# Kernel tuning notes

Hardware: AMD Instinct MI355X
Metric: run time of the kernel (lower is better)

## Reference

```python
import jax, jax.numpy as jnp
import numpy as np
from jax import lax

D_MODEL = 1024
D_STATE = 16


def setup_inputs() -> dict:
    key = jax.random.key(0)
    ks = jax.random.split(key, 7)
    B, L = 4, 2048
    x = jax.random.normal(ks[0], (B, L, D_MODEL), dtype=jnp.float32)
    s = 1.0 / np.sqrt(D_MODEL)
    W_dt = jax.random.uniform(ks[1], (D_MODEL, D_MODEL), jnp.float32, -s, s)
    b_dt = jax.random.uniform(ks[2], (D_MODEL,), jnp.float32, -s, s)
    W_B = jax.random.uniform(ks[3], (D_STATE, D_MODEL), jnp.float32, -s, s)
    W_C = jax.random.uniform(ks[4], (D_STATE, D_MODEL), jnp.float32, -s, s)
    A = jax.random.normal(ks[5], (D_MODEL, D_STATE), dtype=jnp.float32)
    A_log = jnp.log(jnp.abs(A) + 1e-4)
    D = jnp.ones((D_MODEL,), dtype=jnp.float32)
    return {"x": x, "W_dt": W_dt, "b_dt": b_dt, "W_B": W_B, "W_C": W_C,
            "A_log": A_log, "D": D}


def reference(x, W_dt, b_dt, W_B, W_C, A_log, D):
    B, L, Dm = x.shape
    N = A_log.shape[1]
    dt = jax.nn.softplus(jnp.einsum('bld,ed->ble', x, W_dt) + b_dt)  # [B,L,D]
    Bp = jnp.einsum('bld,nd->bln', x, W_B)   # [B,L,N]
    Cp = jnp.einsum('bld,nd->bln', x, W_C)   # [B,L,N]
    A = -jnp.exp(A_log)                      # [D,N]
    dA = jnp.exp(dt[..., None] * A)          # [B,L,D,N]
    # fuse dB * x: dB[bldn] = dt*Bp; input term = dB * x
    dBx = dt[..., None] * Bp[:, :, None, :] * x[..., None]  # [B,L,D,N]

    def step(h, inp):
        dA_t, dBx_t, C_t, x_t = inp
        h = dA_t * h + dBx_t                              # [B,D,N]
        y = jnp.einsum('bdn,bn->bd', h, C_t) + D * x_t    # [B,D]
        return h, y

    h0 = jnp.zeros((B, Dm, N), dtype=x.dtype)
    xs = (jnp.swapaxes(dA, 0, 1), jnp.swapaxes(dBx, 0, 1),
          jnp.swapaxes(Cp, 0, 1), jnp.swapaxes(x, 0, 1))
    _, ys = lax.scan(step, h0, xs)           # ys: [L,B,D]
    return jnp.swapaxes(ys, 0, 1)            # [B,L,D]
```

## Files before the change

### kernel.cpp

```cpp
#include <hip/hip_runtime.h>
#include <hip/hip_bf16.h>
#include <math.h>

#define DM 1024
#define DS 16
#define BB 4
#define LL 2048
#define LC 32
#define NC (LL/LC)
#define MT 8192
#define NT64 16
#define NCT 17

typedef __attribute__((ext_vector_type(8))) short short8;
typedef __attribute__((ext_vector_type(4))) float floatx4;

__device__ __forceinline__ float softplus_fast(float v) {
  return fmaxf(v, 0.f) + __logf(1.f + __expf(-fabsf(v)));
}

__global__ __launch_bounds__(256) void convert_kernel(
    const float* __restrict__ X, const float* __restrict__ W_dt,
    const float* __restrict__ WB, const float* __restrict__ WC,
    __hip_bfloat16* __restrict__ Xb, __hip_bfloat16* __restrict__ Wx)
{
  const size_t i  = (size_t)blockIdx.x * 256 + threadIdx.x;
  const size_t NX = (size_t)MT * DM / 8;
  const size_t NW = (size_t)DM * DM / 8;
  const size_t NB = (size_t)DS * DM / 8;
  const float* src;
  __hip_bfloat16* dst;
  size_t u;
  if (i < NX)                { src = X;    dst = Xb;                        u = i; }
  else if (i < NX + NW)      { src = W_dt; dst = Wx;                        u = i - NX; }
  else if (i < NX + NW + NB) { src = WB;   dst = Wx + (size_t)1024 * DM;    u = i - NX - NW; }
  else if (i < NX + NW + 2 * NB) { src = WC; dst = Wx + (size_t)1040 * DM;  u = i - NX - NW - NB; }
  else {
    const size_t z = i - NX - NW - 2 * NB;
    const short8 zz = {0, 0, 0, 0, 0, 0, 0, 0};
    *(short8*)&Wx[(size_t)1056 * DM + z * 8] = zz;
    return;
  }
  const float4 a = *(const float4*)&src[u * 8];
  const float4 b = *(const float4*)&src[u * 8 + 4];
  union { short8 v; __hip_bfloat16 h[8]; } o;
  o.h[0] = __float2bfloat16(a.x); o.h[1] = __float2bfloat16(a.y);
  o.h[2] = __float2bfloat16(a.z); o.h[3] = __float2bfloat16(a.w);
  o.h[4] = __float2bfloat16(b.x); o.h[5] = __float2bfloat16(b.y);
  o.h[6] = __float2bfloat16(b.z); o.h[7] = __float2bfloat16(b.w);
  *(short8*)&dst[u * 8] = o.v;
}

__global__ __launch_bounds__(256) void gemm_dt_mfma(
    const __hip_bfloat16* __restrict__ Xb, const __hip_bfloat16* __restrict__ Wx,
    const float* __restrict__ bias, __hip_bfloat16* __restrict__ DTb,
    float* __restrict__ BP, float* __restrict__ CP)
{
  __shared__ short As[3][128 * 64];
  __shared__ short Bs[3][64 * 64];
  const int tid  = threadIdx.x;
  const int lane = tid & 63;
  const int wid  = tid >> 6;
  const int wm   = wid >> 1, wn = wid & 1;

  const int bid  = blockIdx.x;
  const int tile = (bid & 7) * 136 + (bid >> 3);
  const int row0 = (tile / NCT) * 128;
  const int col0 = (tile % NCT) * 64;

  const floatx4 zero = {0.f, 0.f, 0.f, 0.f};
  floatx4 acc[4][2];
#pragma unroll
  for (int i = 0; i < 4; ++i)
#pragma unroll
    for (int j = 0; j < 2; ++j) acc[i][j] = zero;

  auto STAGE = [&](int buf, int t) {
    const int k0 = t * 64;
#pragma unroll
    for (int q = 0; q < 4; ++q) {
      const int fe = q * 256 + tid;
      const int r  = fe >> 3;
      const int kk = (fe & 7) ^ (r & 7);
      __builtin_amdgcn_global_load_lds(
          (const __attribute__((address_space(1))) void*)&Xb[(size_t)(row0 + r) * DM + k0 + kk * 8],
          (__attribute__((address_space(3))) void*)&As[buf][fe * 8], 16, 0, 0);
    }
#pragma unroll
    for (int q = 0; q < 2; ++q) {
      const int fe = q * 256 + tid;
      const int r  = fe >> 3;
      const int kk = (fe & 7) ^ (r & 7);
      __builtin_amdgcn_global_load_lds(
          (const __attribute__((address_space(1))) void*)&Wx[(size_t)(col0 + r) * DM + k0 + kk * 8],
          (__attribute__((address_space(3))) void*)&Bs[buf][fe * 8], 16, 0, 0);
    }
  };

  const int fr = lane & 15;
  const int ks = lane >> 4;

  STAGE(0, 0);
  STAGE(1, 1);
  int cur = 0;
  for (int t = 0; t < NT64; ++t) {
    if (t < NT64 - 1) asm volatile("s_waitcnt vmcnt(6)" ::: "memory");
    else              asm volatile("s_waitcnt vmcnt(0)" ::: "memory");
    __builtin_amdgcn_s_barrier();
    __builtin_amdgcn_sched_barrier(0);

    int c2 = cur + 2; if (c2 >= 3) c2 -= 3;
    if (t + 2 < NT64) STAGE(c2, t + 2);

    short8 af[4][2], bfr[2][2];
#pragma unroll
    for (int i = 0; i < 4; ++i) {
      const int ar = wm * 64 + i * 16 + fr;
#pragma unroll
      for (int s = 0; s < 2; ++s) {
        const int ch = (ks + 4 * s) ^ (ar & 7);
        af[i][s] = *(const short8*)&As[cur][ar * 64 + ch * 8];
      }
    }
#pragma unroll
    for (int j = 0; j < 2; ++j) {
      const int br = wn * 32 + j * 16 + fr;
#pragma unroll
      for (int s = 0; s < 2; ++s) {
        const int ch = (ks + 4 * s) ^ (br & 7);
        bfr[j][s] = *(const short8*)&Bs[cur][br * 64 + ch * 8];
      }
    }
#pragma unroll
    for (int s = 0; s < 2; ++s)
#pragma unroll
      for (int i = 0; i < 4; ++i)
#pragma unroll
        for (int j = 0; j < 2; ++j)
          acc[i][j] = __builtin_amdgcn_mfma_f32_16x16x32_bf16(af[i][s], bfr[j][s], acc[i][j], 0, 0, 0);

    cur += 1; if (cur >= 3) cur -= 3;
  }

  const int cl = lane & 15;
  const int rg = lane >> 4;
  if (col0 < 1024) {
#pragma unroll
    for (int i = 0; i < 4; ++i) {
#pragma unroll
      for (int r = 0; r < 4; ++r) {
        const size_t row = (size_t)(row0 + wm * 64 + i * 16 + rg * 4 + r);
#pragma unroll
        for (int j = 0; j < 2; ++j) {
          const int col = col0 + wn * 32 + j * 16 + cl;
          const float v = acc[i][j][r] + bias[col];
          DTb[row * DM + col] = __float2bfloat16(softplus_fast(v));
        }
      }
    }
  } else if (wn == 0) {
#pragma unroll
    for (int i = 0; i < 4; ++i) {
#pragma unroll
      for (int r = 0; r < 4; ++r) {
        const size_t row = (size_t)(row0 + wm * 64 + i * 16 + rg * 4 + r);
        BP[row * DS + cl] = acc[i][0][r];
        CP[row * DS + cl] = acc[i][1][r];
      }
    }
  }
}

__global__ __launch_bounds__(256) void scan_partial_kernel(
    const __hip_bfloat16* __restrict__ DT, const __hip_bfloat16* __restrict__ X,
    const float* __restrict__ Bp, const float* __restrict__ A_log,
    float* __restrict__ SD, float* __restrict__ HP)
{
  const int d = blockIdx.x * 256 + threadIdx.x;
  const int c = blockIdx.y;
  const int b = blockIdx.z;
  float A[DS], h[DS];
  float sdt = 0.f;
  const float4* arow = (const float4*)&A_log[(size_t)d * DS];
#pragma unroll
  for (int m = 0; m < 4; ++m) {
    const float4 a4 = arow[m];
    A[m*4+0] = -__expf(a4.x); A[m*4+1] = -__expf(a4.y);
    A[m*4+2] = -__expf(a4.z); A[m*4+3] = -__expf(a4.w);
  }
#pragma unroll
  for (int n = 0; n < DS; ++n) h[n] = 0.f;

  const int l0 = c * LC;
  size_t idx = ((size_t)b * LL + l0) * DM + d;
  const float4* bv = (const float4*)&Bp[((size_t)b * LL + l0) * DS];

  float dtb[4], xb[4];
#pragma unroll
  for (int u = 0; u < 4; ++u) {
    dtb[u] = __bfloat162float(DT[idx + (size_t)u * DM]);
    xb[u]  = __bfloat162float(X[idx + (size_t)u * DM]);
  }

  for (int l = 0; l < LC; l += 4) {
    float dtn[4], xn[4];
    if (l + 4 < LC) {
#pragma unroll
      for (int u = 0; u < 4; ++u) {
        dtn[u] = __bfloat162float(DT[idx + (size_t)(u + 4) * DM]);
        xn[u]  = __bfloat162float(X[idx + (size_t)(u + 4) * DM]);
      }
    }
#pragma unroll
    for (int u = 0; u < 4; ++u) {
      const float dtv = dtb[u], xv = xb[u];
      const float dx = dtv * xv;
      sdt += dtv;
      const float4 b0 = bv[(l+u)*4+0], b1 = bv[(l+u)*4+1];
      const float4 b2 = bv[(l+u)*4+2], b3 = bv[(l+u)*4+3];
      const float bb[DS] = {b0.x,b0.y,b0.z,b0.w, b1.x,b1.y,b1.z,b1.w,
                            b2.x,b2.y,b2.z,b2.w, b3.x,b3.y,b3.z,b3.w};
#pragma unroll
      for (int n = 0; n < DS; ++n) {
        const float dA = __expf(dtv * A[n]);
        h[n] = fmaf(dA, h[n], dx * bb[n]);
      }
    }
    idx += (size_t)4 * DM;
#pragma unroll
    for (int u = 0; u < 4; ++u) { dtb[u] = dtn[u]; xb[u] = xn[u]; }
  }
  SD[((size_t)b * NC + c) * DM + d] = sdt;
  const size_t o = (((size_t)b * NC + c) * DM + d) * DS;
  float4* hp = (float4*)&HP[o];
#pragma unroll
  for (int m = 0; m < 4; ++m)
    hp[m] = make_float4(h[m*4+0], h[m*4+1], h[m*4+2], h[m*4+3]);
}

__global__ __launch_bounds__(256) void combine_kernel(
    const float* __restrict__ SD, const float* __restrict__ A_log,
    float* HP)
{
  const int idx = blockIdx.x * 256 + threadIdx.x;
  const int b  = idx >> 14;
  const int dn = idx & 16383;
  const int d  = dn >> 4;
  const float A = -__expf(A_log[dn]);
  float h = 0.f;
#pragma unroll 4
  for (int c = 0; c < NC; ++c) {
    const size_t o = (((size_t)b * NC + c) << 14) + dn;
    const float p  = __expf(SD[((size_t)b * NC + c) * DM + d] * A);
    const float hp = HP[o];
    HP[o] = h;
    h = fmaf(p, h, hp);
  }
}

__global__ __launch_bounds__(256) void scan_final_kernel(
    const __hip_bfloat16* __restrict__ DT, const __hip_bfloat16* __restrict__ X,
    const float* __restrict__ Bp, const float* __restrict__ Cp,
    const float* __restrict__ A_log, const float* __restrict__ Dvec,
    const float* __restrict__ Hin, float* __restrict__ Y)
{
  const int d = blockIdx.x * 256 + threadIdx.x;
  const int c = blockIdx.y;
  const int b = blockIdx.z;
  float A[DS], h[DS];
  const float4* arow = (const float4*)&A_log[(size_t)d * DS];
  const size_t o = (((size_t)b * NC + c) * DM + d) * DS;
  const float4* hin = (const float4*)&Hin[o];
#pragma unroll
  for (int m = 0; m < 4; ++m) {
    const float4 a4 = arow[m];
    A[m*4+0] = -__expf(a4.x); A[m*4+1] = -__expf(a4.y);
    A[m*4+2] = -__expf(a4.z); A[m*4+3] = -__expf(a4.w);
    const float4 h4 = hin[m];
    h[m*4+0] = h4.x; h[m*4+1] = h4.y; h[m*4+2] = h4.z; h[m*4+3] = h4.w;
  }
  const float Dd = Dvec[d];
  const int l0 = c * LC;
  size_t idx = ((size_t)b * LL + l0) * DM + d;
  const float4* bv = (const float4*)&Bp[((size_t)b * LL + l0) * DS];
  const float4* cv = (const float4*)&Cp[((size_t)b * LL + l0) * DS];

  float dtb[4], xb[4];
#pragma unroll
  for (int u = 0; u < 4; ++u) {
    dtb[u] = __bfloat162float(DT[idx + (size_t)u * DM]);
    xb[u]  = __bfloat162float(X[idx + (size_t)u * DM]);
  }

  for (int l = 0; l < LC; l += 4) {
    float dtn[4], xn[4];
    if (l + 4 < LC) {
#pragma unroll
      for (int u = 0; u < 4; ++u) {
        dtn[u] = __bfloat162float(DT[idx + (size_t)(u + 4) * DM]);
        xn[u]  = __bfloat162float(X[idx + (size_t)(u + 4) * DM]);
      }
    }
#pragma unroll
    for (int u = 0; u < 4; ++u) {
      const float dtv = dtb[u], xv = xb[u];
      const float dx = dtv * xv;
      const float4 b0 = bv[(l+u)*4+0], b1 = bv[(l+u)*4+1];
      const float4 b2 = bv[(l+u)*4+2], b3 = bv[(l+u)*4+3];
      const float bb[DS] = {b0.x,b0.y,b0.z,b0.w, b1.x,b1.y,b1.z,b1.w,
                            b2.x,b2.y,b2.z,b2.w, b3.x,b3.y,b3.z,b3.w};
      const float4 c0 = cv[(l+u)*4+0], c1 = cv[(l+u)*4+1];
      const float4 c2 = cv[(l+u)*4+2], c3 = cv[(l+u)*4+3];
      const float cc[DS] = {c0.x,c0.y,c0.z,c0.w, c1.x,c1.y,c1.z,c1.w,
                            c2.x,c2.y,c2.z,c2.w, c3.x,c3.y,c3.z,c3.w};
      float y = 0.f;
#pragma unroll
      for (int n = 0; n < DS; ++n) {
        const float dA = __expf(dtv * A[n]);
        h[n] = fmaf(dA, h[n], dx * bb[n]);
        y = fmaf(h[n], cc[n], y);
      }
      Y[idx + (size_t)u * DM] = fmaf(Dd, xv, y);
    }
    idx += (size_t)4 * DM;
#pragma unroll
    for (int u = 0; u < 4; ++u) { dtb[u] = dtn[u]; xb[u] = xn[u]; }
  }
}

extern "C" void kernel_launch(void* const* d_in, const int* in_sizes, int n_in,
                              void* d_out, int out_size, void* d_ws, size_t ws_size,
                              hipStream_t stream)
{
  const float* x     = (const float*)d_in[0];
  const float* W_dt  = (const float*)d_in[1];
  const float* b_dt  = (const float*)d_in[2];
  const float* W_B   = (const float*)d_in[3];
  const float* W_C   = (const float*)d_in[4];
  const float* A_log = (const float*)d_in[5];
  const float* Dv    = (const float*)d_in[6];
  float* Y  = (float*)d_out;
  float* ws = (float*)d_ws;

  __hip_bfloat16* DTb = (__hip_bfloat16*)ws;
  float* BP = ws + (size_t)MT * DM / 2;
  float* CP = BP + (size_t)MT * DS;
  __hip_bfloat16* Xb = (__hip_bfloat16*)(CP + (size_t)MT * DS);
  __hip_bfloat16* Wx = (__hip_bfloat16*)(CP + (size_t)MT * DS + (size_t)MT * DM / 2);
  float* SD = CP + (size_t)MT * DS + (size_t)MT * DM / 2 + (size_t)1088 * DM / 2;
  float* HP = SD + (size_t)BB * NC * DM;

  convert_kernel<<<4640, 256, 0, stream>>>(x, W_dt, W_B, W_C, Xb, Wx);
  gemm_dt_mfma<<<1088, 256, 0, stream>>>(Xb, Wx, b_dt, DTb, BP, CP);
  scan_partial_kernel<<<dim3(DM / 256, NC, BB), 256, 0, stream>>>(DTb, Xb, BP, A_log, SD, HP);
  combine_kernel<<<(BB * DM * DS) / 256, 256, 0, stream>>>(SD, A_log, HP);
  scan_final_kernel<<<dim3(DM / 256, NC, BB), 256, 0, stream>>>(DTb, Xb, BP, CP, A_log, Dv, HP, Y);
}
```

Baseline: 128.4 us.

## Use double buffering in dt GEMM and stage B/C projections in LDS for scans

The GEMM moves from a three-stage buffer with explicit vmcnt waits to a simpler two-buffer scheme with __syncthreads between iterations. This lowers LDS use but shortens the prefetch distance and relies on __syncthreads to drain the async LDS loads. The two scan kernels now copy each chunk's B and C projections into shared memory once, instead of every thread reading the same values through global/scalar loads. The cost is one extra barrier per scan block.

Measured after the change: 117.1 us. -8.9%, faster.

```diff
diff --git a/kernel.cpp b/kernel.cpp
--- a/kernel.cpp
+++ b/kernel.cpp
@@ -56,8 +56,8 @@
     const float* __restrict__ bias, __hip_bfloat16* __restrict__ DTb,
     float* __restrict__ BP, float* __restrict__ CP)
 {
-  __shared__ short As[3][128 * 64];
-  __shared__ short Bs[3][64 * 64];
+  __shared__ short As[2][128 * 64];
+  __shared__ short Bs[2][64 * 64];
   const int tid  = threadIdx.x;
   const int lane = tid & 63;
   const int wid  = tid >> 6;
@@ -101,16 +101,11 @@
   const int ks = lane >> 4;
 
   STAGE(0, 0);
-  STAGE(1, 1);
+  __syncthreads();
+
   int cur = 0;
   for (int t = 0; t < NT64; ++t) {
-    if (t < NT64 - 1) asm volatile("s_waitcnt vmcnt(6)" ::: "memory");
-    else              asm volatile("s_waitcnt vmcnt(0)" ::: "memory");
-    __builtin_amdgcn_s_barrier();
-    __builtin_amdgcn_sched_barrier(0);
-
-    int c2 = cur + 2; if (c2 >= 3) c2 -= 3;
-    if (t + 2 < NT64) STAGE(c2, t + 2);
+    if (t + 1 < NT64) STAGE(cur ^ 1, t + 1);
 
     short8 af[4][2], bfr[2][2];
 #pragma unroll
@@ -139,7 +134,10 @@
         for (int j = 0; j < 2; ++j)
           acc[i][j] = __builtin_amdgcn_mfma_f32_16x16x32_bf16(af[i][s], bfr[j][s], acc[i][j], 0, 0, 0);
 
-    cur += 1; if (cur >= 3) cur -= 3;
+    if (t + 1 < NT64) {
+      __syncthreads();
+      cur ^= 1;
+    }
   }
 
   const int cl = lane & 15;
@@ -176,9 +174,16 @@
     const float* __restrict__ Bp, const float* __restrict__ A_log,
     float* __restrict__ SD, float* __restrict__ HP)
 {
-  const int d = blockIdx.x * 256 + threadIdx.x;
+  __shared__ float sB[LC * DS];
+  const int tid = threadIdx.x;
+  const int d = blockIdx.x * 256 + tid;
   const int c = blockIdx.y;
   const int b = blockIdx.z;
+  const int l0 = c * LC;
+
+  if (tid < LC * DS / 4)
+    ((float4*)sB)[tid] = ((const float4*)&Bp[((size_t)b * LL + l0) * DS])[tid];
+
   float A[DS], h[DS];
   float sdt = 0.f;
   const float4* arow = (const float4*)&A_log[(size_t)d * DS];
@@ -191,16 +196,14 @@
 #pragma unroll
   for (int n = 0; n < DS; ++n) h[n] = 0.f;
 
-  const int l0 = c * LC;
   size_t idx = ((size_t)b * LL + l0) * DM + d;
-  const float4* bv = (const float4*)&Bp[((size_t)b * LL + l0) * DS];
-
   float dtb[4], xb[4];
 #pragma unroll
   for (int u = 0; u < 4; ++u) {
     dtb[u] = __bfloat162float(DT[idx + (size_t)u * DM]);
     xb[u]  = __bfloat162float(X[idx + (size_t)u * DM]);
   }
+  __syncthreads();
 
   for (int l = 0; l < LC; l += 4) {
     float dtn[4], xn[4];
@@ -216,8 +219,10 @@
       const float dtv = dtb[u], xv = xb[u];
       const float dx = dtv * xv;
       sdt += dtv;
-      const float4 b0 = bv[(l+u)*4+0], b1 = bv[(l+u)*4+1];
-      const float4 b2 = bv[(l+u)*4+2], b3 = bv[(l+u)*4+3];
+      const float4 b0 = ((const float4*)sB)[(l+u)*4+0];
+      const float4 b1 = ((const float4*)sB)[(l+u)*4+1];
+      const float4 b2 = ((const float4*)sB)[(l+u)*4+2];
+      const float4 b3 = ((const float4*)sB)[(l+u)*4+3];
       const float bb[DS] = {b0.x,b0.y,b0.z,b0.w, b1.x,b1.y,b1.z,b1.w,
                             b2.x,b2.y,b2.z,b2.w, b3.x,b3.y,b3.z,b3.w};
 #pragma unroll
@@ -264,9 +269,16 @@
     const float* __restrict__ A_log, const float* __restrict__ Dvec,
     const float* __restrict__ Hin, float* __restrict__ Y)
 {
-  const int d = blockIdx.x * 256 + threadIdx.x;
+  __shared__ float sB[LC * DS], sC[LC * DS];
+  const int tid = threadIdx.x;
+  const int d = blockIdx.x * 256 + tid;
   const int c = blockIdx.y;
   const int b = blockIdx.z;
+  const int l0 = c * LC;
+
+  if (tid < 128)       ((float4*)sB)[tid] = ((const float4*)&Bp[((size_t)b * LL + l0) * DS])[tid];
+  else                 ((float4*)sC)[tid - 128] = ((const float4*)&Cp[((size_t)b * LL + l0) * DS])[tid - 128];
+
   float A[DS], h[DS];
   const float4* arow = (const float4*)&A_log[(size_t)d * DS];
   const size_t o = (((size_t)b * NC + c) * DM + d) * DS;
@@ -280,10 +292,7 @@
     h[m*4+0] = h4.x; h[m*4+1] = h4.y; h[m*4+2] = h4.z; h[m*4+3] = h4.w;
   }
   const float Dd = Dvec[d];
-  const int l0 = c * LC;
   size_t idx = ((size_t)b * LL + l0) * DM + d;
-  const float4* bv = (const float4*)&Bp[((size_t)b * LL + l0) * DS];
-  const float4* cv = (const float4*)&Cp[((size_t)b * LL + l0) * DS];
 
   float dtb[4], xb[4];
 #pragma unroll
@@ -291,6 +300,7 @@
     dtb[u] = __bfloat162float(DT[idx + (size_t)u * DM]);
     xb[u]  = __bfloat162float(X[idx + (size_t)u * DM]);
   }
+  __syncthreads();
 
   for (int l = 0; l < LC; l += 4) {
     float dtn[4], xn[4];
@@ -305,12 +315,16 @@
     for (int u = 0; u < 4; ++u) {
       const float dtv = dtb[u], xv = xb[u];
       const float dx = dtv * xv;
-      const float4 b0 = bv[(l+u)*4+0], b1 = bv[(l+u)*4+1];
-      const float4 b2 = bv[(l+u)*4+2], b3 = bv[(l+u)*4+3];
+      const float4 b0 = ((const float4*)sB)[(l+u)*4+0];
+      const float4 b1 = ((const float4*)sB)[(l+u)*4+1];
+      const float4 b2 = ((const float4*)sB)[(l+u)*4+2];
+      const float4 b3 = ((const float4*)sB)[(l+u)*4+3];
       const float bb[DS] = {b0.x,b0.y,b0.z,b0.w, b1.x,b1.y,b1.z,b1.w,
                             b2.x,b2.y,b2.z,b2.w, b3.x,b3.y,b3.z,b3.w};
-      const float4 c0 = cv[(l+u)*4+0], c1 = cv[(l+u)*4+1];
-      const float4 c2 = cv[(l+u)*4+2], c3 = cv[(l+u)*4+3];
+      const float4 c0 = ((const float4*)sC)[(l+u)*4+0];
+      const float4 c1 = ((const float4*)sC)[(l+u)*4+1];
+      const float4 c2 = ((const float4*)sC)[(l+u)*4+2];
+      const float4 c3 = ((const float4*)sC)[(l+u)*4+3];
       const float cc[DS] = {c0.x,c0.y,c0.z,c0.w, c1.x,c1.y,c1.z,c1.w,
                             c2.x,c2.y,c2.z,c2.w, c3.x,c3.y,c3.z,c3.w};
       float y = 0.f;
```
